# Performance work log

Measured on AMD Instinct MI355X. Metric: run time of the kernel, lower is better.

The kernel has to match this reference:

```python
import jax, jax.numpy as jnp
import numpy as np

N = 100000
E = 1600000
G = 100
HEADS = 4
CH = 32
POS = 16
IN_DIM = 128
OUT_DIM = 64
NEG_SLOPE = 0.2
BN_EPS = 1e-5


def _grid_positions(batch):
    # replicate _get_normalized_positions: per-graph ceil(sqrt(count)) grid, vectorized
    counts = jax.ops.segment_sum(jnp.ones(N, jnp.int32), batch, num_segments=G)
    starts = jnp.concatenate([jnp.zeros(1, jnp.int32), jnp.cumsum(counts)[:-1].astype(jnp.int32)])
    local = jnp.arange(N, dtype=jnp.int32) - starts[batch]
    cnt = counts[batch]
    gs = jnp.ceil(jnp.sqrt(cnt.astype(jnp.float32))).astype(jnp.int32)
    row = local // gs
    col = local % gs
    denom = jnp.maximum(gs - 1, 1).astype(jnp.float32)
    return jnp.stack([row.astype(jnp.float32) / denom, col.astype(jnp.float32) / denom], axis=1)


def _seg_softmax(alpha, dst):
    # numerically-stable softmax over edges grouped by destination node
    amax = jax.ops.segment_max(alpha, dst, num_segments=N)
    amax = jnp.where(jnp.isfinite(amax), amax, 0.0)
    e = jnp.exp(alpha - amax[dst])
    s = jax.ops.segment_sum(e, dst, num_segments=N)
    return e / (s[dst] + 1e-16)


def _gat_layer(h, pos, src, dst, W, att, Wp, b):
    xt = (h @ W.T).reshape(N, HEADS, CH)                       # [N,H,C]
    pe = (pos[dst] - pos[src]) @ Wp.T                          # [E',P]
    a = att[0]                                                 # [H, 2C+P]
    # decompose (cat(x_src, x_dst, pe) * att).sum(-1) to avoid [E',H,2C+P] intermediate
    a_src = jnp.einsum('nhc,hc->nh', xt, a[:, :CH])
    a_dst = jnp.einsum('nhc,hc->nh', xt, a[:, CH:2 * CH])
    alpha = a_src[src] + a_dst[dst] + pe @ a[:, 2 * CH:].T     # [E',H]
    alpha = jnp.where(alpha > 0, alpha, NEG_SLOPE * alpha)     # leaky_relu
    alpha = _seg_softmax(alpha, dst)
    # faithful to source: message uses x[dst_idx], aggregated onto dst
    out = jax.ops.segment_sum(xt[dst] * alpha[:, :, None], dst, num_segments=N)
    return out.reshape(N, HEADS * CH) + b


def _batchnorm(h, g, b):
    mu = h.mean(0)
    var = h.var(0)  # biased, matches torch BN training-mode normalization
    return (h - mu) / jnp.sqrt(var + BN_EPS) * g + b


def setup_inputs() -> dict:
    key = jax.random.key(0)
    ks = jax.random.split(key, 20)
    s = 0.1
    return {
        'x': jax.random.normal(ks[0], (N, IN_DIM), jnp.float32),
        'edge_index': jax.random.randint(ks[1], (2, E), 0, N, jnp.int32),
        'batch': (jnp.arange(N, dtype=jnp.int32) // (N // G)).astype(jnp.int32),
        'pe_W': jax.random.normal(ks[2], (POS, 2), jnp.float32) * s,
        'pe_b': jax.random.normal(ks[3], (POS,), jnp.float32) * s,
        'lin_W0': jax.random.normal(ks[4], (HEADS * CH, IN_DIM + POS), jnp.float32) * s,
        'att0': jax.random.normal(ks[5], (1, HEADS, 2 * CH + POS), jnp.float32) * s,
        'posW0': jax.random.normal(ks[6], (POS, 2), jnp.float32) * s,
        'bias0': jax.random.normal(ks[7], (HEADS * CH,), jnp.float32) * s,
        'bn_g0': jax.random.uniform(ks[8], (HEADS * CH,), jnp.float32, 0.5, 1.5),
        'bn_b0': jax.random.normal(ks[9], (HEADS * CH,), jnp.float32) * s,
        'lin_W1': jax.random.normal(ks[10], (HEADS * CH, HEADS * CH), jnp.float32) * s,
        'att1': jax.random.normal(ks[11], (1, HEADS, 2 * CH + POS), jnp.float32) * s,
        'posW1': jax.random.normal(ks[12], (POS, 2), jnp.float32) * s,
        'bias1': jax.random.normal(ks[13], (HEADS * CH,), jnp.float32) * s,
        'bn_g1': jax.random.uniform(ks[14], (HEADS * CH,), jnp.float32, 0.5, 1.5),
        'bn_b1': jax.random.normal(ks[15], (HEADS * CH,), jnp.float32) * s,
        'fc_W': jax.random.normal(ks[16], (OUT_DIM, HEADS * CH), jnp.float32) * s,
        'fc_b': jax.random.normal(ks[17], (OUT_DIM,), jnp.float32) * s,
    }


def reference(x, edge_index, batch, pe_W, pe_b,
              lin_W0, att0, posW0, bias0, bn_g0, bn_b0,
              lin_W1, att1, posW1, bias1, bn_g1, bn_b1,
              fc_W, fc_b):
    pos = _grid_positions(batch)
    h = jnp.concatenate([x, pos @ pe_W.T + pe_b], axis=1)      # PositionalEncoding
    loop = jnp.arange(N, dtype=edge_index.dtype)
    src = jnp.concatenate([edge_index[0], loop])               # add_self_loops
    dst = jnp.concatenate([edge_index[1], loop])
    layers = ((lin_W0, att0, posW0, bias0, bn_g0, bn_b0),
              (lin_W1, att1, posW1, bias1, bn_g1, bn_b1))
    for (W, att, Wp, b, g, bb) in layers:
        h = _gat_layer(h, pos, src, dst, W, att, Wp, b)
        h = _batchnorm(h, g, bb)
        h = jax.nn.elu(h)
        # dropout: eval mode (identity); _refine_positions is identity
    counts = jax.ops.segment_sum(jnp.ones(N, jnp.float32), batch, num_segments=G)
    pooled = jax.ops.segment_sum(h, batch, num_segments=G) / counts[:, None]
    return pooled @ fc_W.T + fc_b
```

## Files before the change

### kernel.cpp

```cpp
#include <hip/hip_runtime.h>

#define NN 100000

typedef __bf16 bf16x8 __attribute__((ext_vector_type(8)));
typedef float  f32x4  __attribute__((ext_vector_type(4)));

__device__ __forceinline__ float b2f(ushort u) {
    union { unsigned int i; float f; } v; v.i = ((unsigned int)u) << 16; return v.f;
}
__device__ __forceinline__ ushort f2b(float f) {
    union { float f; unsigned int i; } v; v.f = f;
    unsigned int r = (v.i + 0x7fffu + ((v.i >> 16) & 1u)) >> 16;
    return (ushort)r;
}
__device__ __forceinline__ float elu_f(float v) {
    return v > 0.0f ? v : __expf(v) - 1.0f;
}

__global__ __launch_bounds__(256)
void zero_k(const float* __restrict__ W0, const float* __restrict__ W1,
            float* __restrict__ stats, float* __restrict__ out,
            ushort* __restrict__ wb0, ushort* __restrict__ wb1) {
    int i = blockIdx.x * 256 + threadIdx.x;
    if (i < 14592) { if (i < 8192) stats[i] = 0.0f; else out[i - 8192] = 0.0f; }
    if (i < 18432) wb0[i] = f2b(W0[i]);
    else if (i < 34816) wb1[i - 18432] = f2b(W1[i - 18432]);
}

template<int KK, int KP, bool FIRST>
__global__ __launch_bounds__(256, 4)
void gemm_k(const void* __restrict__ Av, const ushort* __restrict__ Wb,
            const float* __restrict__ peW, const float* __restrict__ peB,
            const float* __restrict__ statsIn, const float* __restrict__ g,
            const float* __restrict__ bb, ushort* __restrict__ Z,
            float* __restrict__ statsOut)
{
    constexpr int NKC = KP / 32;
    __shared__ ushort ZS[64 * 136];
    __shared__ float smS[256], smQ[256];
    __shared__ float smSS[256];
    const int t = threadIdx.x;
    const int blockM = blockIdx.x * 64;

    const int wave = t >> 6, lane = t & 63;
    const int wm = (wave & 1) * 32, wn = (wave >> 1) * 64;
    const int m = lane & 15, kq = lane >> 4;

    bf16x8 af[2][NKC];
    if constexpr (FIRST) {
        const float* A = (const float*)Av;
        #pragma unroll
        for (int mi = 0; mi < 2; ++mi) {
            const int gr = blockM + wm + mi * 16 + m;
            const bool ok = gr < NN;
            #pragma unroll
            for (int kc = 0; kc < 4; ++kc) {
                const int k0 = kc * 32 + kq * 8;
                float4 v0 = make_float4(0.f, 0.f, 0.f, 0.f), v1 = v0;
                if (ok) {
                    v0 = *(const float4*)(A + (size_t)gr * 128 + k0);
                    v1 = *(const float4*)(A + (size_t)gr * 128 + k0 + 4);
                }
                ushort u[8] = { f2b(v0.x), f2b(v0.y), f2b(v0.z), f2b(v0.w),
                                f2b(v1.x), f2b(v1.y), f2b(v1.z), f2b(v1.w) };
                af[mi][kc] = *(bf16x8*)u;
            }
            {
                ushort u[8] = {0, 0, 0, 0, 0, 0, 0, 0};
                if (kq < 2 && ok) {
                    const int local = gr - (gr / 1000) * 1000;
                    const float px = (float)(local >> 5) * (1.0f / 31.0f);
                    const float py = (float)(local & 31) * (1.0f / 31.0f);
                    #pragma unroll
                    for (int j = 0; j < 8; ++j) {
                        int p = kq * 8 + j;
                        u[j] = f2b(px * peW[2 * p] + py * peW[2 * p + 1] + peB[p]);
                    }
                }
                af[mi][NKC - 1] = *(bf16x8*)u;
            }
        }
    } else {
        const ushort* A = (const ushort*)Av;
        uint4 raw[2][4];
        #pragma unroll
        for (int mi = 0; mi < 2; ++mi) {
            const int gr = blockM + wm + mi * 16 + m;
            const bool ok = gr < NN;
            #pragma unroll
            for (int kc = 0; kc < 4; ++kc) {
                raw[mi][kc] = make_uint4(0u, 0u, 0u, 0u);
                if (ok) raw[mi][kc] = *(const uint4*)(A + (size_t)gr * 128 + kc * 32 + kq * 8);
            }
        }
        if (t < 128) {
            float S = 0.f, Q = 0.f;
            #pragma unroll
            for (int k = 0; k < 16; ++k) {
                S += statsIn[k * 256 + t]; Q += statsIn[k * 256 + 128 + t];
            }
            float mu = S * (1.0f / NN);
            float var = fmaxf(Q * (1.0f / NN) - mu * mu, 0.0f);
            float istd = rsqrtf(var + 1e-5f);
            float sc = g[t] * istd;
            smSS[t] = sc; smSS[128 + t] = bb[t] - mu * sc;
        }
        __syncthreads();
        #pragma unroll
        for (int mi = 0; mi < 2; ++mi) {
            const bool ok = (blockM + wm + mi * 16 + m) < NN;
            #pragma unroll
            for (int kc = 0; kc < 4; ++kc) {
                const int k0 = kc * 32 + kq * 8;
                ushort* u = (ushort*)&raw[mi][kc];
                #pragma unroll
                for (int j = 0; j < 8; ++j) {
                    float val = b2f(u[j]) * smSS[k0 + j] + smSS[128 + k0 + j];
                    u[j] = ok ? f2b(elu_f(val)) : (ushort)0;
                }
                af[mi][kc] = *(bf16x8*)&raw[mi][kc];
            }
        }
    }

    f32x4 acc[2][4];
    #pragma unroll
    for (int mi = 0; mi < 2; ++mi)
        #pragma unroll
        for (int ni = 0; ni < 4; ++ni)
            acc[mi][ni] = (f32x4){0.0f, 0.0f, 0.0f, 0.0f};

    #pragma unroll
    for (int kc = 0; kc < NKC; ++kc) {
        const int k0 = kc * 32 + kq * 8;
        bf16x8 bf[4];
        #pragma unroll
        for (int ni = 0; ni < 4; ++ni) {
            if (KP == KK || k0 < KK)
                bf[ni] = *(const bf16x8*)(Wb + (wn + ni * 16 + m) * KK + k0);
            else {
                ushort z[8] = {0, 0, 0, 0, 0, 0, 0, 0};
                bf[ni] = *(bf16x8*)z;
            }
        }
        #pragma unroll
        for (int mi = 0; mi < 2; ++mi)
            #pragma unroll
            for (int ni = 0; ni < 4; ++ni)
                acc[mi][ni] = __builtin_amdgcn_mfma_f32_16x16x32_bf16(
                    af[mi][kc], bf[ni], acc[mi][ni], 0, 0, 0);
    }

    float s[4] = {0, 0, 0, 0}, q[4] = {0, 0, 0, 0};
    #pragma unroll
    for (int mi = 0; mi < 2; ++mi)
        #pragma unroll
        for (int ni = 0; ni < 4; ++ni)
            #pragma unroll
            for (int r = 0; r < 4; ++r) {
                const float z = acc[mi][ni][r];
                s[ni] += z; q[ni] += z * z;
            }
    #pragma unroll
    for (int ni = 0; ni < 4; ++ni) {
        s[ni] += __shfl_xor(s[ni], 16); s[ni] += __shfl_xor(s[ni], 32);
        q[ni] += __shfl_xor(q[ni], 16); q[ni] += __shfl_xor(q[ni], 32);
    }
    if (lane < 16) {
        #pragma unroll
        for (int ni = 0; ni < 4; ++ni) {
            const int idx = wave * 64 + ni * 16 + m;
            smS[idx] = s[ni]; smQ[idx] = q[ni];
        }
    }
    #pragma unroll
    for (int mi = 0; mi < 2; ++mi)
        #pragma unroll
        for (int ni = 0; ni < 4; ++ni) {
            const int col = wn + ni * 16 + m;
            const int rb = wm + mi * 16 + kq * 4;
            #pragma unroll
            for (int r = 0; r < 4; ++r)
                ZS[(rb + r) * 136 + col] = f2b(acc[mi][ni][r]);
        }
    __syncthreads();

    if (t < 128) {
        const int base = (t >> 6) * 128 + (t & 63);
        float S = smS[base] + smS[base + 64];
        float Q = smQ[base] + smQ[base + 64];
        float* sl = statsOut + (blockIdx.x & 15) * 256;
        atomicAdd(sl + t, S);
        atomicAdd(sl + 128 + t, Q);
    }
    #pragma unroll
    for (int i = 0; i < 4; ++i) {
        const int idx = i * 256 + t;
        const int row = idx >> 4, c16 = idx & 15;
        const int gr = blockM + row;
        if (gr < NN)
            *(uint4*)(Z + (size_t)gr * 128 + c16 * 8) =
                *(const uint4*)(ZS + row * 136 + c16 * 8);
    }
}

__global__ __launch_bounds__(256)
void poolfc_k(const ushort* __restrict__ Z, const float* __restrict__ stats,
              const float* __restrict__ g, const float* __restrict__ bb,
              const float* __restrict__ fcW, const float* __restrict__ fcB,
              float* __restrict__ out) {
    __shared__ float smSS[256];
    __shared__ float smT[16 * 128];
    __shared__ float smP[128];
    const int t = threadIdx.x;
    if (t < 128) {
        float S = 0.f, Q = 0.f;
        #pragma unroll
        for (int k = 0; k < 16; ++k) { S += stats[k * 256 + t]; Q += stats[k * 256 + 128 + t]; }
        float mu = S * (1.0f / NN);
        float var = fmaxf(Q * (1.0f / NN) - mu * mu, 0.0f);
        float istd = rsqrtf(var + 1e-5f);
        float sc = g[t] * istd;
        smSS[t] = sc; smSS[128 + t] = bb[t] - mu * sc;
    }
    __syncthreads();
    const int gg = blockIdx.x >> 2, part = blockIdx.x & 3;
    const int r16 = t >> 4, c8 = t & 15;
    const int r0 = gg * 1000 + part * 250;
    float sc[8], sh[8];
    #pragma unroll
    for (int j = 0; j < 8; ++j) { sc[j] = smSS[c8 * 8 + j]; sh[j] = smSS[128 + c8 * 8 + j]; }
    float a[8] = {0, 0, 0, 0, 0, 0, 0, 0};
    #pragma unroll
    for (int i = 0; i < 16; ++i) {
        if (i < 15 || r16 < 10) {
            const uint4 v = *(const uint4*)(Z + ((size_t)(r0 + i * 16 + r16)) * 128 + c8 * 8);
            const ushort* u = (const ushort*)&v;
            #pragma unroll
            for (int j = 0; j < 8; ++j) a[j] += elu_f(b2f(u[j]) * sc[j] + sh[j]);
        }
    }
    #pragma unroll
    for (int j = 0; j < 8; ++j) smT[r16 * 128 + c8 * 8 + j] = a[j];
    __syncthreads();
    if (t < 128) {
        float S = 0.0f;
        #pragma unroll
        for (int k = 0; k < 16; ++k) S += smT[k * 128 + t];
        smP[t] = S;
    }
    __syncthreads();
    if (t < 64) {
        float d = 0.0f;
        #pragma unroll
        for (int j4 = 0; j4 < 32; ++j4) {
            float4 w = *(const float4*)(fcW + t * 128 + j4 * 4);
            d += smP[j4 * 4 + 0] * w.x + smP[j4 * 4 + 1] * w.y
               + smP[j4 * 4 + 2] * w.z + smP[j4 * 4 + 3] * w.w;
        }
        float acc = d * (1.0f / 1000.0f) + (part == 0 ? fcB[t] : 0.0f);
        atomicAdd(&out[gg * 64 + t], acc);
    }
}

extern "C" void kernel_launch(void* const* d_in, const int* in_sizes, int n_in,
                              void* d_out, int out_size, void* d_ws, size_t ws_size,
                              hipStream_t stream) {
    const float* x   = (const float*)d_in[0];
    const float* peW = (const float*)d_in[3];
    const float* peB = (const float*)d_in[4];
    const float* W0  = (const float*)d_in[5];
    const float* g0  = (const float*)d_in[9];
    const float* bb0 = (const float*)d_in[10];
    const float* W1  = (const float*)d_in[11];
    const float* g1  = (const float*)d_in[15];
    const float* bb1 = (const float*)d_in[16];
    const float* fcW = (const float*)d_in[17];
    const float* fcB = (const float*)d_in[18];
    float* out = (float*)d_out;

    float* wsF = (float*)d_ws;
    float* stats1 = wsF;
    float* stats2 = wsF + 4096;
    ushort* wb0 = (ushort*)((char*)d_ws + 65536);
    ushort* wb1 = (ushort*)((char*)d_ws + 131072);
    ushort* z1 = (ushort*)((char*)d_ws + 262144);
    ushort* z2 = (ushort*)((char*)d_ws + 25862144);

    zero_k<<<136, 256, 0, stream>>>(W0, W1, stats1, out, wb0, wb1);
    gemm_k<144, 160, true ><<<1563, 256, 0, stream>>>(
        (const void*)x, wb0, peW, peB, nullptr, nullptr, nullptr, z1, stats1);
    gemm_k<128, 128, false><<<1563, 256, 0, stream>>>(
        (const void*)z1, wb1, nullptr, nullptr, stats1, g0, bb0, z2, stats2);
    poolfc_k<<<400, 256, 0, stream>>>(z2, stats2, g1, bb1, fcW, fcB, out);
}
```

Baseline: 181.5 us.

## Fuse all stages into one persistent cooperative kernel with grid syncs

Replaces the four separate launches (weight conversion/zeroing, two GEMM+BN passes, pool+FC) with a single cooperative persistent kernel. Blocks loop over tiles and use grid.sync between phases, and each block computes the BN scale/shift once per phase. This removes kernel launch gaps and repeated per-block stats reduction. In exchange it adds grid-wide barrier cost and limits the grid to the resident occupancy, which may reduce latency hiding relative to oversubscribed launches.

```diff
diff --git a/kernel.cpp b/kernel.cpp
--- a/kernel.cpp
+++ b/kernel.cpp
@@ -1,4 +1,7 @@
 #include <hip/hip_runtime.h>
+#include <hip/hip_cooperative_groups.h>
+
+namespace cg = cooperative_groups;
 
 #define NN 100000
 
@@ -17,30 +20,18 @@
     return v > 0.0f ? v : __expf(v) - 1.0f;
 }
 
-__global__ __launch_bounds__(256)
-void zero_k(const float* __restrict__ W0, const float* __restrict__ W1,
-            float* __restrict__ stats, float* __restrict__ out,
-            ushort* __restrict__ wb0, ushort* __restrict__ wb1) {
-    int i = blockIdx.x * 256 + threadIdx.x;
-    if (i < 14592) { if (i < 8192) stats[i] = 0.0f; else out[i - 8192] = 0.0f; }
-    if (i < 18432) wb0[i] = f2b(W0[i]);
-    else if (i < 34816) wb1[i - 18432] = f2b(W1[i - 18432]);
-}
-
 template<int KK, int KP, bool FIRST>
-__global__ __launch_bounds__(256, 4)
-void gemm_k(const void* __restrict__ Av, const ushort* __restrict__ Wb,
-            const float* __restrict__ peW, const float* __restrict__ peB,
-            const float* __restrict__ statsIn, const float* __restrict__ g,
-            const float* __restrict__ bb, ushort* __restrict__ Z,
-            float* __restrict__ statsOut)
+__device__ __forceinline__
+void gemm_tile(const int tile, const void* __restrict__ Av,
+               const ushort* __restrict__ Wb,
+               const float* __restrict__ peW, const float* __restrict__ peB,
+               const float* __restrict__ smSS,
+               ushort* __restrict__ Z, float* __restrict__ statsOut,
+               ushort* ZS, float* smS, float* smQ)
 {
     constexpr int NKC = KP / 32;
-    __shared__ ushort ZS[64 * 136];
-    __shared__ float smS[256], smQ[256];
-    __shared__ float smSS[256];
     const int t = threadIdx.x;
-    const int blockM = blockIdx.x * 64;
+    const int blockM = tile * 64;
 
     const int wave = t >> 6, lane = t & 63;
     const int wm = (wave & 1) * 32, wn = (wave >> 1) * 64;
@@ -93,19 +84,6 @@
                 if (ok) raw[mi][kc] = *(const uint4*)(A + (size_t)gr * 128 + kc * 32 + kq * 8);
             }
         }
-        if (t < 128) {
-            float S = 0.f, Q = 0.f;
-            #pragma unroll
-            for (int k = 0; k < 16; ++k) {
-                S += statsIn[k * 256 + t]; Q += statsIn[k * 256 + 128 + t];
-            }
-            float mu = S * (1.0f / NN);
-            float var = fmaxf(Q * (1.0f / NN) - mu * mu, 0.0f);
-            float istd = rsqrtf(var + 1e-5f);
-            float sc = g[t] * istd;
-            smSS[t] = sc; smSS[128 + t] = bb[t] - mu * sc;
-        }
-        __syncthreads();
         #pragma unroll
         for (int mi = 0; mi < 2; ++mi) {
             const bool ok = (blockM + wm + mi * 16 + m) < NN;
@@ -189,7 +167,7 @@
         const int base = (t >> 6) * 128 + (t & 63);
         float S = smS[base] + smS[base + 64];
         float Q = smQ[base] + smQ[base + 64];
-        float* sl = statsOut + (blockIdx.x & 15) * 256;
+        float* sl = statsOut + (tile & 15) * 256;
         atomicAdd(sl + t, S);
         atomicAdd(sl + 128 + t, Q);
     }
@@ -202,64 +180,104 @@
             *(uint4*)(Z + (size_t)gr * 128 + c16 * 8) =
                 *(const uint4*)(ZS + row * 136 + c16 * 8);
     }
-}
-
-__global__ __launch_bounds__(256)
-void poolfc_k(const ushort* __restrict__ Z, const float* __restrict__ stats,
-              const float* __restrict__ g, const float* __restrict__ bb,
-              const float* __restrict__ fcW, const float* __restrict__ fcB,
-              float* __restrict__ out) {
-    __shared__ float smSS[256];
-    __shared__ float smT[16 * 128];
-    __shared__ float smP[128];
+    __syncthreads();
+}
+
+__global__ __launch_bounds__(256, 4)
+void fused_k(const float* __restrict__ x, const float* __restrict__ W0,
+             const float* __restrict__ W1, const float* __restrict__ peW,
+             const float* __restrict__ peB, const float* __restrict__ g0,
+             const float* __restrict__ bb0, const float* __restrict__ g1,
+             const float* __restrict__ bb1, const float* __restrict__ fcW,
+             const float* __restrict__ fcB, float* __restrict__ out,
+             float* __restrict__ stats1, float* __restrict__ stats2,
+             ushort* __restrict__ wb0, ushort* __restrict__ wb1,
+             ushort* __restrict__ z1, ushort* __restrict__ z2)
+{
+    cg::grid_group grid = cg::this_grid();
+    __shared__ ushort ZS[64 * 136];
+    __shared__ float smS[256], smQ[256], smSS[256];
     const int t = threadIdx.x;
+    const int bid = blockIdx.x;
+    const int nb = gridDim.x;
+
+    for (int i = bid * 256 + t; i < 34816; i += nb * 256) {
+        if (i < 14592) { if (i < 8192) stats1[i] = 0.0f; else out[i - 8192] = 0.0f; }
+        if (i < 18432) wb0[i] = f2b(W0[i]);
+        else wb1[i - 18432] = f2b(W1[i - 18432]);
+    }
+    grid.sync();
+
+    for (int tile = bid; tile < 1563; tile += nb)
+        gemm_tile<144, 160, true>(tile, (const void*)x, wb0, peW, peB, nullptr,
+                                  z1, stats1, ZS, smS, smQ);
+    grid.sync();
+
     if (t < 128) {
         float S = 0.f, Q = 0.f;
         #pragma unroll
-        for (int k = 0; k < 16; ++k) { S += stats[k * 256 + t]; Q += stats[k * 256 + 128 + t]; }
+        for (int k = 0; k < 16; ++k) { S += stats1[k * 256 + t]; Q += stats1[k * 256 + 128 + t]; }
         float mu = S * (1.0f / NN);
         float var = fmaxf(Q * (1.0f / NN) - mu * mu, 0.0f);
-        float istd = rsqrtf(var + 1e-5f);
-        float sc = g[t] * istd;
-        smSS[t] = sc; smSS[128 + t] = bb[t] - mu * sc;
+        float sc = g0[t] * rsqrtf(var + 1e-5f);
+        smSS[t] = sc; smSS[128 + t] = bb0[t] - mu * sc;
     }
     __syncthreads();
-    const int gg = blockIdx.x >> 2, part = blockIdx.x & 3;
+    for (int tile = bid; tile < 1563; tile += nb)
+        gemm_tile<128, 128, false>(tile, (const void*)z1, wb1, nullptr, nullptr, smSS,
+                                   z2, stats2, ZS, smS, smQ);
+    grid.sync();
+
+    if (t < 128) {
+        float S = 0.f, Q = 0.f;
+        #pragma unroll
+        for (int k = 0; k < 16; ++k) { S += stats2[k * 256 + t]; Q += stats2[k * 256 + 128 + t]; }
+        float mu = S * (1.0f / NN);
+        float var = fmaxf(Q * (1.0f / NN) - mu * mu, 0.0f);
+        float sc = g1[t] * rsqrtf(var + 1e-5f);
+        smSS[t] = sc; smSS[128 + t] = bb1[t] - mu * sc;
+    }
+    __syncthreads();
+    float* smT = (float*)ZS;
+    float* smP = (float*)(ZS + 4096);
     const int r16 = t >> 4, c8 = t & 15;
-    const int r0 = gg * 1000 + part * 250;
-    float sc[8], sh[8];
-    #pragma unroll
-    for (int j = 0; j < 8; ++j) { sc[j] = smSS[c8 * 8 + j]; sh[j] = smSS[128 + c8 * 8 + j]; }
-    float a[8] = {0, 0, 0, 0, 0, 0, 0, 0};
-    #pragma unroll
-    for (int i = 0; i < 16; ++i) {
-        if (i < 15 || r16 < 10) {
-            const uint4 v = *(const uint4*)(Z + ((size_t)(r0 + i * 16 + r16)) * 128 + c8 * 8);
-            const ushort* u = (const ushort*)&v;
-            #pragma unroll
-            for (int j = 0; j < 8; ++j) a[j] += elu_f(b2f(u[j]) * sc[j] + sh[j]);
-        }
-    }
-    #pragma unroll
-    for (int j = 0; j < 8; ++j) smT[r16 * 128 + c8 * 8 + j] = a[j];
-    __syncthreads();
-    if (t < 128) {
-        float S = 0.0f;
-        #pragma unroll
-        for (int k = 0; k < 16; ++k) S += smT[k * 128 + t];
-        smP[t] = S;
-    }
-    __syncthreads();
-    if (t < 64) {
-        float d = 0.0f;
-        #pragma unroll
-        for (int j4 = 0; j4 < 32; ++j4) {
-            float4 w = *(const float4*)(fcW + t * 128 + j4 * 4);
-            d += smP[j4 * 4 + 0] * w.x + smP[j4 * 4 + 1] * w.y
-               + smP[j4 * 4 + 2] * w.z + smP[j4 * 4 + 3] * w.w;
-        }
-        float acc = d * (1.0f / 1000.0f) + (part == 0 ? fcB[t] : 0.0f);
-        atomicAdd(&out[gg * 64 + t], acc);
+    float sc8[8], sh8[8];
+    #pragma unroll
+    for (int j = 0; j < 8; ++j) { sc8[j] = smSS[c8 * 8 + j]; sh8[j] = smSS[128 + c8 * 8 + j]; }
+    for (int p = bid; p < 400; p += nb) {
+        const int gg = p >> 2, part = p & 3;
+        const int r0 = gg * 1000 + part * 250;
+        float a[8] = {0, 0, 0, 0, 0, 0, 0, 0};
+        #pragma unroll
+        for (int i = 0; i < 16; ++i) {
+            if (i < 15 || r16 < 10) {
+                const uint4 v = *(const uint4*)(z2 + ((size_t)(r0 + i * 16 + r16)) * 128 + c8 * 8);
+                const ushort* u = (const ushort*)&v;
+                #pragma unroll
+                for (int j = 0; j < 8; ++j) a[j] += elu_f(b2f(u[j]) * sc8[j] + sh8[j]);
+            }
+        }
+        #pragma unroll
+        for (int j = 0; j < 8; ++j) smT[r16 * 128 + c8 * 8 + j] = a[j];
+        __syncthreads();
+        if (t < 128) {
+            float S = 0.0f;
+            #pragma unroll
+            for (int k = 0; k < 16; ++k) S += smT[k * 128 + t];
+            smP[t] = S;
+        }
+        __syncthreads();
+        if (t < 64) {
+            float d = 0.0f;
+            #pragma unroll
+            for (int j4 = 0; j4 < 32; ++j4) {
+                float4 w = *(const float4*)(fcW + t * 128 + j4 * 4);
+                d += smP[j4 * 4 + 0] * w.x + smP[j4 * 4 + 1] * w.y
+                   + smP[j4 * 4 + 2] * w.z + smP[j4 * 4 + 3] * w.w;
+            }
+            atomicAdd(&out[gg * 64 + t], d * (1.0f / 1000.0f) + (part == 0 ? fcB[t] : 0.0f));
+        }
+        __syncthreads();
     }
 }
 
@@ -287,10 +305,18 @@
     ushort* z1 = (ushort*)((char*)d_ws + 262144);
     ushort* z2 = (ushort*)((char*)d_ws + 25862144);
 
-    zero_k<<<136, 256, 0, stream>>>(W0, W1, stats1, out, wb0, wb1);
-    gemm_k<144, 160, true ><<<1563, 256, 0, stream>>>(
-        (const void*)x, wb0, peW, peB, nullptr, nullptr, nullptr, z1, stats1);
-    gemm_k<128, 128, false><<<1563, 256, 0, stream>>>(
-        (const void*)z1, wb1, nullptr, nullptr, stats1, g0, bb0, z2, stats2);
-    poolfc_k<<<400, 256, 0, stream>>>(z2, stats2, g1, bb1, fcW, fcB, out);
-}
+    static int nblocks = 0;
+    if (nblocks == 0) {
+        int per_cu = 0;
+        if (hipOccupancyMaxActiveBlocksPerMultiprocessor(&per_cu, fused_k, 256, 0)
+                != hipSuccess || per_cu < 1)
+            per_cu = 4;
+        long total = (long)per_cu * 256;
+        nblocks = (int)(total > 1563 ? 1563 : total);
+    }
+
+    void* args[] = { &x, &W0, &W1, &peW, &peB, &g0, &bb0, &g1, &bb1, &fcW, &fcB,
+                     &out, &stats1, &stats2, &wb0, &wb1, &z1, &z2 };
+    hipLaunchCooperativeKernel((void*)fused_k, dim3(nblocks), dim3(256),
+                               args, 0, stream);
+}
```

Result: slower. 466.0 us (+156.7%).

## Remap GEMM waves to 16 rows by full 128 columns and double pooling blocks

Applied to the files above, without the earlier changes.

Each wave in the GEMM kernels now computes 16 rows by all 128 output columns, where before it computed a 32x64 sub-tile. Each A row is now loaded and converted by only one wave, so the duplicate global A loads and BN/ELU work across waves go away, at the cost of every wave reading the whole weight matrix. Column-stat partials grow to four per column. The pool+FC kernel is split into 8 parts per graph instead of 4, doubling the grid for more parallelism.

```diff
diff --git a/kernel.cpp b/kernel.cpp
--- a/kernel.cpp
+++ b/kernel.cpp
@@ -37,61 +37,54 @@
 {
     constexpr int NKC = KP / 32;
     __shared__ ushort ZS[64 * 136];
-    __shared__ float smS[256], smQ[256];
+    __shared__ float smS[512], smQ[512];
     __shared__ float smSS[256];
     const int t = threadIdx.x;
     const int blockM = blockIdx.x * 64;
 
     const int wave = t >> 6, lane = t & 63;
-    const int wm = (wave & 1) * 32, wn = (wave >> 1) * 64;
+    const int wm = wave * 16;
     const int m = lane & 15, kq = lane >> 4;
 
-    bf16x8 af[2][NKC];
+    const int gr = blockM + wm + m;
+    const bool ok = gr < NN;
+
+    bf16x8 af[NKC];
     if constexpr (FIRST) {
         const float* A = (const float*)Av;
         #pragma unroll
-        for (int mi = 0; mi < 2; ++mi) {
-            const int gr = blockM + wm + mi * 16 + m;
-            const bool ok = gr < NN;
-            #pragma unroll
-            for (int kc = 0; kc < 4; ++kc) {
-                const int k0 = kc * 32 + kq * 8;
-                float4 v0 = make_float4(0.f, 0.f, 0.f, 0.f), v1 = v0;
-                if (ok) {
-                    v0 = *(const float4*)(A + (size_t)gr * 128 + k0);
-                    v1 = *(const float4*)(A + (size_t)gr * 128 + k0 + 4);
+        for (int kc = 0; kc < 4; ++kc) {
+            const int k0 = kc * 32 + kq * 8;
+            float4 v0 = make_float4(0.f, 0.f, 0.f, 0.f), v1 = v0;
+            if (ok) {
+                v0 = *(const float4*)(A + (size_t)gr * 128 + k0);
+                v1 = *(const float4*)(A + (size_t)gr * 128 + k0 + 4);
+            }
+            ushort u[8] = { f2b(v0.x), f2b(v0.y), f2b(v0.z), f2b(v0.w),
+                            f2b(v1.x), f2b(v1.y), f2b(v1.z), f2b(v1.w) };
+            af[kc] = *(bf16x8*)u;
+        }
+        {
+            ushort u[8] = {0, 0, 0, 0, 0, 0, 0, 0};
+            if (kq < 2 && ok) {
+                const int local = gr - (gr / 1000) * 1000;
+                const float px = (float)(local >> 5) * (1.0f / 31.0f);
+                const float py = (float)(local & 31) * (1.0f / 31.0f);
+                #pragma unroll
+                for (int j = 0; j < 8; ++j) {
+                    int p = kq * 8 + j;
+                    u[j] = f2b(px * peW[2 * p] + py * peW[2 * p + 1] + peB[p]);
                 }
-                ushort u[8] = { f2b(v0.x), f2b(v0.y), f2b(v0.z), f2b(v0.w),
-                                f2b(v1.x), f2b(v1.y), f2b(v1.z), f2b(v1.w) };
-                af[mi][kc] = *(bf16x8*)u;
-            }
-            {
-                ushort u[8] = {0, 0, 0, 0, 0, 0, 0, 0};
-                if (kq < 2 && ok) {
-                    const int local = gr - (gr / 1000) * 1000;
-                    const float px = (float)(local >> 5) * (1.0f / 31.0f);
-                    const float py = (float)(local & 31) * (1.0f / 31.0f);
-                    #pragma unroll
-                    for (int j = 0; j < 8; ++j) {
-                        int p = kq * 8 + j;
-                        u[j] = f2b(px * peW[2 * p] + py * peW[2 * p + 1] + peB[p]);
-                    }
-                }
-                af[mi][NKC - 1] = *(bf16x8*)u;
-            }
+            }
+            af[NKC - 1] = *(bf16x8*)u;
         }
     } else {
         const ushort* A = (const ushort*)Av;
-        uint4 raw[2][4];
-        #pragma unroll
-        for (int mi = 0; mi < 2; ++mi) {
-            const int gr = blockM + wm + mi * 16 + m;
-            const bool ok = gr < NN;
-            #pragma unroll
-            for (int kc = 0; kc < 4; ++kc) {
-                raw[mi][kc] = make_uint4(0u, 0u, 0u, 0u);
-                if (ok) raw[mi][kc] = *(const uint4*)(A + (size_t)gr * 128 + kc * 32 + kq * 8);
-            }
+        uint4 raw[4];
+        #pragma unroll
+        for (int kc = 0; kc < 4; ++kc) {
+            raw[kc] = make_uint4(0u, 0u, 0u, 0u);
+            if (ok) raw[kc] = *(const uint4*)(A + (size_t)gr * 128 + kc * 32 + kq * 8);
         }
         if (t < 128) {
             float S = 0.f, Q = 0.f;
@@ -107,88 +100,81 @@
         }
         __syncthreads();
         #pragma unroll
-        for (int mi = 0; mi < 2; ++mi) {
-            const bool ok = (blockM + wm + mi * 16 + m) < NN;
-            #pragma unroll
-            for (int kc = 0; kc < 4; ++kc) {
-                const int k0 = kc * 32 + kq * 8;
-                ushort* u = (ushort*)&raw[mi][kc];
-                #pragma unroll
-                for (int j = 0; j < 8; ++j) {
-                    float val = b2f(u[j]) * smSS[k0 + j] + smSS[128 + k0 + j];
-                    u[j] = ok ? f2b(elu_f(val)) : (ushort)0;
-                }
-                af[mi][kc] = *(bf16x8*)&raw[mi][kc];
-            }
-        }
-    }
-
-    f32x4 acc[2][4];
-    #pragma unroll
-    for (int mi = 0; mi < 2; ++mi)
-        #pragma unroll
-        for (int ni = 0; ni < 4; ++ni)
-            acc[mi][ni] = (f32x4){0.0f, 0.0f, 0.0f, 0.0f};
+        for (int kc = 0; kc < 4; ++kc) {
+            const int k0 = kc * 32 + kq * 8;
+            ushort* u = (ushort*)&raw[kc];
+            #pragma unroll
+            for (int j = 0; j < 8; ++j) {
+                float val = b2f(u[j]) * smSS[k0 + j] + smSS[128 + k0 + j];
+                u[j] = ok ? f2b(elu_f(val)) : (ushort)0;
+            }
+            af[kc] = *(bf16x8*)&raw[kc];
+        }
+    }
+
+    f32x4 acc[8];
+    #pragma unroll
+    for (int ni = 0; ni < 8; ++ni)
+        acc[ni] = (f32x4){0.0f, 0.0f, 0.0f, 0.0f};
 
     #pragma unroll
     for (int kc = 0; kc < NKC; ++kc) {
         const int k0 = kc * 32 + kq * 8;
-        bf16x8 bf[4];
-        #pragma unroll
-        for (int ni = 0; ni < 4; ++ni) {
-            if (KP == KK || k0 < KK)
-                bf[ni] = *(const bf16x8*)(Wb + (wn + ni * 16 + m) * KK + k0);
-            else {
-                ushort z[8] = {0, 0, 0, 0, 0, 0, 0, 0};
-                bf[ni] = *(bf16x8*)z;
-            }
-        }
-        #pragma unroll
-        for (int mi = 0; mi < 2; ++mi)
-            #pragma unroll
-            for (int ni = 0; ni < 4; ++ni)
-                acc[mi][ni] = __builtin_amdgcn_mfma_f32_16x16x32_bf16(
-                    af[mi][kc], bf[ni], acc[mi][ni], 0, 0, 0);
-    }
-
-    float s[4] = {0, 0, 0, 0}, q[4] = {0, 0, 0, 0};
-    #pragma unroll
-    for (int mi = 0; mi < 2; ++mi)
-        #pragma unroll
-        for (int ni = 0; ni < 4; ++ni)
-            #pragma unroll
-            for (int r = 0; r < 4; ++r) {
-                const float z = acc[mi][ni][r];
-                s[ni] += z; q[ni] += z * z;
-            }
-    #pragma unroll
-    for (int ni = 0; ni < 4; ++ni) {
+        #pragma unroll
+        for (int nh = 0; nh < 2; ++nh) {
+            bf16x8 bf[4];
+            #pragma unroll
+            for (int nj = 0; nj < 4; ++nj) {
+                const int ni = nh * 4 + nj;
+                if (KP == KK || k0 < KK)
+                    bf[nj] = *(const bf16x8*)(Wb + (ni * 16 + m) * KK + k0);
+                else {
+                    ushort z[8] = {0, 0, 0, 0, 0, 0, 0, 0};
+                    bf[nj] = *(bf16x8*)z;
+                }
+            }
+            #pragma unroll
+            for (int nj = 0; nj < 4; ++nj)
+                acc[nh * 4 + nj] = __builtin_amdgcn_mfma_f32_16x16x32_bf16(
+                    af[kc], bf[nj], acc[nh * 4 + nj], 0, 0, 0);
+        }
+    }
+
+    float s[8], q[8];
+    #pragma unroll
+    for (int ni = 0; ni < 8; ++ni) {
+        s[ni] = 0.f; q[ni] = 0.f;
+        #pragma unroll
+        for (int r = 0; r < 4; ++r) {
+            const float z = acc[ni][r];
+            s[ni] += z; q[ni] += z * z;
+        }
+    }
+    #pragma unroll
+    for (int ni = 0; ni < 8; ++ni) {
         s[ni] += __shfl_xor(s[ni], 16); s[ni] += __shfl_xor(s[ni], 32);
         q[ni] += __shfl_xor(q[ni], 16); q[ni] += __shfl_xor(q[ni], 32);
     }
     if (lane < 16) {
         #pragma unroll
-        for (int ni = 0; ni < 4; ++ni) {
-            const int idx = wave * 64 + ni * 16 + m;
+        for (int ni = 0; ni < 8; ++ni) {
+            const int idx = wave * 128 + ni * 16 + m;
             smS[idx] = s[ni]; smQ[idx] = q[ni];
         }
     }
     #pragma unroll
-    for (int mi = 0; mi < 2; ++mi)
-        #pragma unroll
-        for (int ni = 0; ni < 4; ++ni) {
-            const int col = wn + ni * 16 + m;
-            const int rb = wm + mi * 16 + kq * 4;
-            #pragma unroll
-            for (int r = 0; r < 4; ++r)
-                ZS[(rb + r) * 136 + col] = f2b(acc[mi][ni][r]);
-        }
+    for (int ni = 0; ni < 8; ++ni) {
+        const int col = ni * 16 + m;
+        const int rb = wm + kq * 4;
+        #pragma unroll
+        for (int r = 0; r < 4; ++r)
+            ZS[(rb + r) * 136 + col] = f2b(acc[ni][r]);
+    }
     __syncthreads();
 
     if (t < 128) {
-        const int base = (t >> 6) * 128 + (t & 63);
-        float S = smS[base] + smS[base + 64];
-        float Q = smQ[base] + smQ[base + 64];
+        float S = smS[t] + smS[128 + t] + smS[256 + t] + smS[384 + t];
+        float Q = smQ[t] + smQ[128 + t] + smQ[256 + t] + smQ[384 + t];
         float* sl = statsOut + (blockIdx.x & 15) * 256;
         atomicAdd(sl + t, S);
         atomicAdd(sl + 128 + t, Q);
@@ -197,9 +183,9 @@
     for (int i = 0; i < 4; ++i) {
         const int idx = i * 256 + t;
         const int row = idx >> 4, c16 = idx & 15;
-        const int gr = blockM + row;
-        if (gr < NN)
-            *(uint4*)(Z + (size_t)gr * 128 + c16 * 8) =
+        const int grr = blockM + row;
+        if (grr < NN)
+            *(uint4*)(Z + (size_t)grr * 128 + c16 * 8) =
                 *(const uint4*)(ZS + row * 136 + c16 * 8);
     }
 }
@@ -224,16 +210,16 @@
         smSS[t] = sc; smSS[128 + t] = bb[t] - mu * sc;
     }
     __syncthreads();
-    const int gg = blockIdx.x >> 2, part = blockIdx.x & 3;
+    const int gg = blockIdx.x >> 3, part = blockIdx.x & 7;
     const int r16 = t >> 4, c8 = t & 15;
-    const int r0 = gg * 1000 + part * 250;
+    const int r0 = gg * 1000 + part * 125;
     float sc[8], sh[8];
     #pragma unroll
     for (int j = 0; j < 8; ++j) { sc[j] = smSS[c8 * 8 + j]; sh[j] = smSS[128 + c8 * 8 + j]; }
     float a[8] = {0, 0, 0, 0, 0, 0, 0, 0};
     #pragma unroll
-    for (int i = 0; i < 16; ++i) {
-        if (i < 15 || r16 < 10) {
+    for (int i = 0; i < 8; ++i) {
+        if (i < 7 || r16 < 13) {
             const uint4 v = *(const uint4*)(Z + ((size_t)(r0 + i * 16 + r16)) * 128 + c8 * 8);
             const ushort* u = (const ushort*)&v;
             #pragma unroll
@@ -292,5 +278,5 @@
         (const void*)x, wb0, peW, peB, nullptr, nullptr, nullptr, z1, stats1);
     gemm_k<128, 128, false><<<1563, 256, 0, stream>>>(
         (const void*)z1, wb1, nullptr, nullptr, stats1, g0, bb0, z2, stats2);
-    poolfc_k<<<400, 256, 0, stream>>>(z2, stats2, g1, bb1, fcW, fcB, out);
-}
+    poolfc_k<<<800, 256, 0, stream>>>(z2, stats2, g1, bb1, fcW, fcB, out);
+}
```

Measured after the change: 194.7 us. 7.2% more time.
